# Kernel optimization log

Measured on AMD Instinct MI355X. Metric: run time of the kernel, lower is better.

Reference implementation:

```python
import jax, jax.numpy as jnp
import numpy as np

B, T, KD, QD, AD, VD, W = 16, 4096, 1024, 1024, 512, 1024, 8


def moving_sum(x, back, forward):
    # x: [B, T] -> windowed sum over [t-back, t+forward], matches F.conv1d with ones filter
    xp = jnp.pad(x, ((0, 0), (back, forward)))[:, None, :]
    filt = jnp.ones((1, 1, back + forward + 1), x.dtype)
    y = jax.lax.conv_general_dilated(xp, filt, (1,), 'VALID')
    return y[:, 0, :]


def setup_inputs() -> dict:
    key = jax.random.key(0)
    ks = jax.random.split(key, 16)
    inp = {
        'key': jax.random.normal(ks[0], (B, T, KD), jnp.float32),
        'value': jax.random.normal(ks[1], (B, T, VD), jnp.float32),
        'query': jax.random.normal(ks[2], (B, 1, QD), jnp.float32),
        'noise': jax.random.normal(ks[3], (B, T), jnp.float32),
        'Wk_mono': jax.random.normal(ks[4], (KD, AD), jnp.float32) * (KD ** -0.5),
        'b_mono': jnp.zeros((AD,), jnp.float32),
        'Wq_mono': jax.random.normal(ks[5], (QD, AD), jnp.float32) * (QD ** -0.5),
        'Wk_chunk': jax.random.normal(ks[6], (KD, AD), jnp.float32) * (KD ** -0.5),
        'b_chunk': jnp.zeros((AD,), jnp.float32),
        'Wq_chunk': jax.random.normal(ks[7], (QD, AD), jnp.float32) * (QD ** -0.5),
        'r_mono': jnp.array([-4.0], jnp.float32),
        'r_chunk': jnp.array([-4.0], jnp.float32),
    }
    # weight-normalized v vectors: g = sqrt(1/attn_dim), w = g * v/||v||
    g = (1.0 / AD) ** 0.5
    vm = jax.random.normal(ks[8], (AD,), jnp.float32)
    vc = jax.random.normal(ks[9], (AD,), jnp.float32)
    inp['v_mono'] = g * vm / jnp.linalg.norm(vm)
    inp['v_chunk'] = g * vc / jnp.linalg.norm(vc)
    return inp


def _forward(key, value, query, noise, Wk_mono, b_mono, Wq_mono, v_mono, r_mono,
             Wk_chunk, b_chunk, Wq_chunk, v_chunk, r_chunk):
    bs, kmax = key.shape[0], key.shape[1]
    # aw_prev default: one-hot at position 0
    aw_prev = jnp.zeros((bs, kmax), key.dtype).at[:, 0].set(1.0)

    # monotonic energy: [B, T]
    qm = jnp.einsum('bqd,da->bqa', query, Wq_mono)  # [B,1,A], broadcasts over T
    e_mono = jnp.einsum('bta,a->bt', jnp.tanh(key @ Wk_mono + b_mono + qm), v_mono) + r_mono

    # parallel mode: sigmoid with additive gaussian noise
    p_choose = jax.nn.sigmoid(e_mono + noise)
    # safe_cumprod with the original's exclusive_cumsum (prepends ONES, drops last)
    log1mp = jnp.log(jnp.clip(1.0 - p_choose, 1e-10, 1.0))
    shifted = jnp.concatenate([jnp.ones((bs, 1), key.dtype), log1mp[:, :-1]], axis=1)
    cumprod_1mp = jnp.exp(jnp.cumsum(shifted, axis=1))
    aw = p_choose * cumprod_1mp * jnp.cumsum(
        aw_prev / jnp.clip(cumprod_1mp, 1e-10, 1.0), axis=1)

    # chunk energy
    qc = jnp.einsum('bqd,da->bqa', query, Wq_chunk)
    e_chunk = jnp.einsum('bta,a->bt', jnp.tanh(key @ Wk_chunk + b_chunk + qc), v_chunk) + r_chunk

    # efficient chunkwise attention
    u = e_chunk - jnp.max(e_chunk, axis=1, keepdims=True)
    softmax_exp = jnp.maximum(jnp.exp(u), 1e-5)
    denom = moving_sum(softmax_exp, back=W - 1, forward=0)
    beta = softmax_exp * moving_sum(aw / denom, back=0, forward=W - 1)

    cv = jnp.einsum('bt,btd->bd', beta, value)[:, None, :]  # [B,1,VD]
    return cv, aw[..., None]


def reference(key, value, query, noise, Wk_mono, b_mono, Wq_mono, v_mono, r_mono,
              Wk_chunk, b_chunk, Wq_chunk, v_chunk, r_chunk):
    return _forward(key, value, query, noise, Wk_mono, b_mono, Wq_mono, v_mono, r_mono,
                    Wk_chunk, b_chunk, Wq_chunk, v_chunk, r_chunk)
```

## Files before the change

### kernel.cpp

```cpp
#include <hip/hip_runtime.h>
#include <hip/hip_bf16.h>
#include <math.h>

#define B_   16
#define T_   4096
#define KD_  1024
#define AD_  512
#define VD_  1024

typedef float f32x4 __attribute__((ext_vector_type(4)));
typedef short s16x8 __attribute__((ext_vector_type(8)));

static __device__ __forceinline__ short f2bf(float f) {
    __hip_bfloat16 h = __float2bfloat16(f);
    return __builtin_bit_cast(short, h);
}

static __device__ __forceinline__ float fast_tanh(float x) {
    x = fminf(fmaxf(x, -15.f), 15.f);
    float e = __expf(2.f * x);
    return (e - 1.f) / (e + 1.f);
}

static __device__ __forceinline__ void gload16(const void* g, void* l) {
    __builtin_amdgcn_global_load_lds(
        (const __attribute__((address_space(1))) void*)(g),
        (__attribute__((address_space(3))) void*)(l), 16, 0, 0);
}


__global__ __launch_bounds__(256) void cvt_key_blk_kernel(
    const float* __restrict__ key, short* __restrict__ keyB) {
    const size_t nchunk = (size_t)B_ * T_ * KD_ / 8;
    size_t stride = (size_t)gridDim.x * 256;
    for (size_t g = (size_t)blockIdx.x * 256 + threadIdx.x; g < nchunk; g += stride) {
        const float* p = key + g * 8;
        f32x4 f0 = *reinterpret_cast<const f32x4*>(p);
        f32x4 f1 = *reinterpret_cast<const f32x4*>(p + 4);
        s16x8 h;
        h[0] = f2bf(f0[0]); h[1] = f2bf(f0[1]); h[2] = f2bf(f0[2]); h[3] = f2bf(f0[3]);
        h[4] = f2bf(f1[0]); h[5] = f2bf(f1[1]); h[6] = f2bf(f1[2]); h[7] = f2bf(f1[3]);
        size_t m = g >> 7;
        int kc = (int)(g & 127);
        size_t mt = m >> 7;
        int r = (int)(m & 127);
        int kt = kc >> 2;
        int sub = kc & 3;
        int c = (r << 2) | (sub ^ ((r >> 1) & 3));
        *reinterpret_cast<s16x8*>(keyB + (((mt * 32 + kt) * 512 + c) << 3)) = h;
    }
}

__global__ __launch_bounds__(256) void qproj_kernel(
    const float* __restrict__ query,
    const float* __restrict__ Wq_mono, const float* __restrict__ b_mono,
    const float* __restrict__ Wq_chunk, const float* __restrict__ b_chunk,
    float* __restrict__ qb) {
    __shared__ float red[4][64];
    int b = blockIdx.x;
    int mat = blockIdx.y;
    int ac = blockIdx.z;
    const float* Wq = mat ? Wq_chunk : Wq_mono;
    const float* bb = mat ? b_chunk : b_mono;
    int al = threadIdx.x & 63;
    int dg = threadIdx.x >> 6;
    int a = ac * 64 + al;
    const float* q = query + b * KD_ + dg * 256;
    const float* wp = Wq + (size_t)(dg * 256) * AD_ + a;
    float s = 0.f;
#pragma unroll 4
    for (int d = 0; d < 256; ++d)
        s += q[d] * wp[(size_t)d * AD_];
    red[dg][al] = s;
    __syncthreads();
    if (dg == 0) {
        float t = red[0][al] + red[1][al] + red[2][al] + red[3][al];
        qb[(mat * B_ + b) * AD_ + a] = t + bb[a];
    }
}

__global__ __launch_bounds__(256) void wtrans_kernel(
    const float* __restrict__ Wk_mono, const float* __restrict__ Wk_chunk,
    short* __restrict__ WkT, short* __restrict__ WkTB) {
    __shared__ float tile[32][33];
    int n0 = blockIdx.x * 32;
    int k0 = blockIdx.y * 32;
    int tx = threadIdx.x;
    int ty = threadIdx.y;
    int tid = ty * 32 + tx;
    const float* src;
    int nloc;
    if (n0 < 512) { src = Wk_mono;  nloc = n0; }
    else          { src = Wk_chunk; nloc = n0 - 512; }
#pragma unroll
    for (int i = 0; i < 4; ++i) {
        int k = ty + i * 8;
        tile[k][tx] = src[(size_t)(k0 + k) * AD_ + nloc + tx];
    }
    __syncthreads();
#pragma unroll
    for (int i = 0; i < 4; ++i) {
        int r = ty + i * 8;
        WkT[(size_t)(n0 + r) * KD_ + k0 + tx] = f2bf(tile[tx][r]);
    }
    if (tid < 128) {
        int r = tid >> 2;
        int sub = tid & 3;
        s16x8 h;
#pragma unroll
        for (int j = 0; j < 8; ++j)
            h[j] = f2bf(tile[sub * 8 + j][r]);
        int n = n0 + r;
        int nblk = n >> 7;
        int rloc = n & 127;
        int kt = k0 >> 5;
        int c = (rloc << 2) | (sub ^ ((rloc >> 1) & 3));
        *reinterpret_cast<s16x8*>(WkTB + (((size_t)(nblk * 32 + kt) * 512 + c) << 3)) = h;
    }
}

__global__ __launch_bounds__(256) void gemm_e_bf_kernel(
    const short* __restrict__ keyB,
    const short* __restrict__ WkTB,
    const float* __restrict__ qb,
    const float* __restrict__ v_mono, const float* __restrict__ v_chunk,
    float* __restrict__ e_ws ) {
    __shared__ short As[2][128 * 32];
    __shared__ short Bs[2][128 * 32];
    int tid = threadIdx.x;
    int bid = blockIdx.x;
    int swz = (bid & 7) * 512 + (bid >> 3);
    int mt = swz >> 3;
    int nt = swz & 7;
    int mBase = mt * 128;
    int nBase = nt * 128;
    int lane = tid & 63;
    int wid = tid >> 6;
    int wr = wid >> 1, wc = wid & 1;
    int col16 = lane & 15, g4 = lane >> 4;

    int c0 = wid * 128 + lane;
    int c1 = c0 + 64;
    const short* pA0 = keyB + (((size_t)mt * 32) * 512 + c0) * 8;
    const short* pA1 = keyB + (((size_t)mt * 32) * 512 + c1) * 8;
    const short* pB0 = WkTB + (((size_t)nt * 32) * 512 + c0) * 8;
    const short* pB1 = WkTB + (((size_t)nt * 32) * 512 + c1) * 8;
    int sOff0 = (wid * 128 + 0) * 8;
    int sOff1 = (wid * 128 + 64) * 8;

    int aoff[4], boff[4];
#pragma unroll
    for (int m = 0; m < 4; ++m) {
        int row = wr * 64 + m * 16 + col16;
        aoff[m] = (row * 4 + (g4 ^ ((row >> 1) & 3))) * 8;
    }
#pragma unroll
    for (int n = 0; n < 4; ++n) {
        int row = wc * 64 + n * 16 + col16;
        boff[n] = (row * 4 + (g4 ^ ((row >> 1) & 3))) * 8;
    }

    f32x4 zero4 = {0.f, 0.f, 0.f, 0.f};
    f32x4 acc[4][4];
#pragma unroll
    for (int m = 0; m < 4; ++m)
#pragma unroll
        for (int n = 0; n < 4; ++n) acc[m][n] = zero4;

    gload16(pA0, &As[0][sOff0]);
    gload16(pA1, &As[0][sOff1]);
    gload16(pB0, &Bs[0][sOff0]);
    gload16(pB1, &Bs[0][sOff1]);
    pA0 += 4096; pA1 += 4096; pB0 += 4096; pB1 += 4096;
    __syncthreads();

    int cur = 0;
    for (int kt = 0; kt < 31; ++kt) {
        int nxt = cur ^ 1;
        gload16(pA0, &As[nxt][sOff0]);
        gload16(pA1, &As[nxt][sOff1]);
        gload16(pB0, &Bs[nxt][sOff0]);
        gload16(pB1, &Bs[nxt][sOff1]);
        pA0 += 4096; pA1 += 4096; pB0 += 4096; pB1 += 4096;
        s16x8 af[4], bfr[4];
#pragma unroll
        for (int m = 0; m < 4; ++m)
            af[m] = *reinterpret_cast<const s16x8*>(&As[cur][aoff[m]]);
#pragma unroll
        for (int n = 0; n < 4; ++n)
            bfr[n] = *reinterpret_cast<const s16x8*>(&Bs[cur][boff[n]]);
#pragma unroll
        for (int m = 0; m < 4; ++m)
#pragma unroll
            for (int n = 0; n < 4; ++n)
                acc[m][n] = __builtin_amdgcn_mfma_f32_16x16x32_bf16(af[m], bfr[n], acc[m][n], 0, 0, 0);
        __syncthreads();
        cur = nxt;
    }
    {
        s16x8 af[4], bfr[4];
#pragma unroll
        for (int m = 0; m < 4; ++m)
            af[m] = *reinterpret_cast<const s16x8*>(&As[cur][aoff[m]]);
#pragma unroll
        for (int n = 0; n < 4; ++n)
            bfr[n] = *reinterpret_cast<const s16x8*>(&Bs[cur][boff[n]]);
#pragma unroll
        for (int m = 0; m < 4; ++m)
#pragma unroll
            for (int n = 0; n < 4; ++n)
                acc[m][n] = __builtin_amdgcn_mfma_f32_16x16x32_bf16(af[m], bfr[n], acc[m][n], 0, 0, 0);
    }

    int bIdx = mBase >> 12;
    int matrix = nBase >> 9;
    int aBase = (nBase & 511) + wc * 64 + col16;
    const float* qbRow = qb + (matrix * B_ + bIdx) * AD_;
    const float* vv = matrix ? v_chunk : v_mono;
    float* eArr = e_ws + matrix * (B_ * T_);
    float qcol[4], vcol[4];
#pragma unroll
    for (int n = 0; n < 4; ++n) {
        int a = aBase + n * 16;
        qcol[n] = qbRow[a];
        vcol[n] = vv[a];
    }
#pragma unroll
    for (int m = 0; m < 4; ++m) {
        float s0 = 0.f, s1 = 0.f, s2 = 0.f, s3 = 0.f;
#pragma unroll
        for (int n = 0; n < 4; ++n) {
            s0 += fast_tanh(acc[m][n][0] + qcol[n]) * vcol[n];
            s1 += fast_tanh(acc[m][n][1] + qcol[n]) * vcol[n];
            s2 += fast_tanh(acc[m][n][2] + qcol[n]) * vcol[n];
            s3 += fast_tanh(acc[m][n][3] + qcol[n]) * vcol[n];
        }
#pragma unroll
        for (int mask = 1; mask < 16; mask <<= 1) {
            s0 += __shfl_xor(s0, mask, 64);
            s1 += __shfl_xor(s1, mask, 64);
            s2 += __shfl_xor(s2, mask, 64);
            s3 += __shfl_xor(s3, mask, 64);
        }
        if (col16 == 0) {
            int rowB = mBase + wr * 64 + m * 16 + g4 * 4;
            atomicAdd(&eArr[rowB + 0], s0);
            atomicAdd(&eArr[rowB + 1], s1);
            atomicAdd(&eArr[rowB + 2], s2);
            atomicAdd(&eArr[rowB + 3], s3);
        }
    }
}

__global__ __launch_bounds__(256) void gemm_e_f32a_kernel(
    const float* __restrict__ key,
    const short* __restrict__ WkT,
    const float* __restrict__ qb,
    const float* __restrict__ v_mono, const float* __restrict__ v_chunk,
    float* __restrict__ e_ws) {
    __shared__ short As[128][40];
    __shared__ short Bs[128][40];
    int tid = threadIdx.x;
    int bid = blockIdx.x;
    int mt = bid >> 3;
    int nt = bid & 7;
    int mBase = mt * 128;
    int nBase = nt * 128;
    int lane = tid & 63;
    int wid = tid >> 6;
    int wr = wid >> 1, wc = wid & 1;
    int col16 = lane & 15, g4 = lane >> 4;

    f32x4 zero4 = {0.f, 0.f, 0.f, 0.f};
    f32x4 acc[4][4];
#pragma unroll
    for (int m = 0; m < 4; ++m)
#pragma unroll
        for (int n = 0; n < 4; ++n) acc[m][n] = zero4;

    for (int kt = 0; kt < 32; ++kt) {
        int k0 = kt * 32;
#pragma unroll
        for (int c2 = 0; c2 < 2; ++c2) {
            int c = c2 * 256 + tid;
            int row = c >> 2;
            int kk = (c & 3) * 8;
            const float* srcA = key + (size_t)(mBase + row) * KD_ + k0 + kk;
            f32x4 f0 = *reinterpret_cast<const f32x4*>(srcA);
            f32x4 f1 = *reinterpret_cast<const f32x4*>(srcA + 4);
            s16x8 h;
            h[0] = f2bf(f0[0]); h[1] = f2bf(f0[1]); h[2] = f2bf(f0[2]); h[3] = f2bf(f0[3]);
            h[4] = f2bf(f1[0]); h[5] = f2bf(f1[1]); h[6] = f2bf(f1[2]); h[7] = f2bf(f1[3]);
            *reinterpret_cast<s16x8*>(&As[row][kk]) = h;
            const short* srcB = WkT + (size_t)(nBase + row) * KD_ + k0 + kk;
            *reinterpret_cast<s16x8*>(&Bs[row][kk]) = *reinterpret_cast<const s16x8*>(srcB);
        }
        __syncthreads();
        s16x8 af[4], bfr[4];
#pragma unroll
        for (int m = 0; m < 4; ++m)
            af[m] = *reinterpret_cast<const s16x8*>(&As[wr * 64 + m * 16 + col16][g4 * 8]);
#pragma unroll
        for (int n = 0; n < 4; ++n)
            bfr[n] = *reinterpret_cast<const s16x8*>(&Bs[wc * 64 + n * 16 + col16][g4 * 8]);
#pragma unroll
        for (int m = 0; m < 4; ++m)
#pragma unroll
            for (int n = 0; n < 4; ++n)
                acc[m][n] = __builtin_amdgcn_mfma_f32_16x16x32_bf16(af[m], bfr[n], acc[m][n], 0, 0, 0);
        __syncthreads();
    }

    int bIdx = mBase >> 12;
    int matrix = nBase >> 9;
    int aBase = (nBase & 511) + wc * 64 + col16;
    const float* qbRow = qb + (matrix * B_ + bIdx) * AD_;
    const float* vv = matrix ? v_chunk : v_mono;
    float* eArr = e_ws + matrix * (B_ * T_);
    float qcol[4], vcol[4];
#pragma unroll
    for (int n = 0; n < 4; ++n) {
        int a = aBase + n * 16;
        qcol[n] = qbRow[a];
        vcol[n] = vv[a];
    }
#pragma unroll
    for (int m = 0; m < 4; ++m) {
        float s0 = 0.f, s1 = 0.f, s2 = 0.f, s3 = 0.f;
#pragma unroll
        for (int n = 0; n < 4; ++n) {
            s0 += fast_tanh(acc[m][n][0] + qcol[n]) * vcol[n];
            s1 += fast_tanh(acc[m][n][1] + qcol[n]) * vcol[n];
            s2 += fast_tanh(acc[m][n][2] + qcol[n]) * vcol[n];
            s3 += fast_tanh(acc[m][n][3] + qcol[n]) * vcol[n];
        }
#pragma unroll
        for (int mask = 1; mask < 16; mask <<= 1) {
            s0 += __shfl_xor(s0, mask, 64);
            s1 += __shfl_xor(s1, mask, 64);
            s2 += __shfl_xor(s2, mask, 64);
            s3 += __shfl_xor(s3, mask, 64);
        }
        if (col16 == 0) {
            int rowB = mBase + wr * 64 + m * 16 + g4 * 4;
            atomicAdd(&eArr[rowB + 0], s0);
            atomicAdd(&eArr[rowB + 1], s1);
            atomicAdd(&eArr[rowB + 2], s2);
            atomicAdd(&eArr[rowB + 3], s3);
        }
    }
}

__global__ __launch_bounds__(256) void scan_kernel(
    const float* __restrict__ e_ws,
    const float* __restrict__ noise,
    const float* __restrict__ r_mono, const float* __restrict__ r_chunk,
    float* __restrict__ aw_out, float* __restrict__ beta_out) {
    __shared__ float s_aw[T_];
    __shared__ float s_sexp[T_];
    __shared__ float s_ad[T_];
    __shared__ float s_w[4];
    int b = blockIdx.x;
    int tid = threadIdx.x;
    int lane = tid & 63;
    int wid4 = tid >> 6;
    int t0 = tid * 16;
    const float* em = e_ws + b * T_;
    const float* ec = e_ws + B_ * T_ + b * T_;
    const float* nz = noise + b * T_;
    float rm = r_mono[0], rc = r_chunk[0];

    float pv[16], lp[16];
    float run = 0.f;
#pragma unroll
    for (int j = 0; j < 16; ++j) {
        float x = em[t0 + j] + rm + nz[t0 + j];
        float p = 1.f / (1.f + expf(-x));
        pv[j] = p;
        float om = fminf(fmaxf(1.f - p, 1e-10f), 1.f);
        lp[j] = run;
        run += logf(om);
    }
    float x = run;
#pragma unroll
    for (int off = 1; off < 64; off <<= 1) {
        float y = __shfl_up(x, off, 64);
        if (lane >= off) x += y;
    }
    if (lane == 63) s_w[wid4] = x;
    __syncthreads();
    float wbase = 0.f;
#pragma unroll
    for (int i = 0; i < 3; ++i) if (i < wid4) wbase += s_w[i];
    float base = 1.f + (wbase + x - run);
#pragma unroll
    for (int j = 0; j < 16; ++j) {
        float aw = pv[j] * expf(base + lp[j]);
        s_aw[t0 + j] = aw;
        aw_out[b * T_ + t0 + j] = aw;
    }
    float evs[16];
    float lmax = -INFINITY;
#pragma unroll
    for (int j = 0; j < 16; ++j) {
        float v = ec[t0 + j] + rc;
        evs[j] = v;
        lmax = fmaxf(lmax, v);
    }
#pragma unroll
    for (int off = 1; off < 64; off <<= 1)
        lmax = fmaxf(lmax, __shfl_xor(lmax, off, 64));
    __syncthreads();
    if (lane == 0) s_w[wid4] = lmax;
    __syncthreads();
    float mx = fmaxf(fmaxf(s_w[0], s_w[1]), fmaxf(s_w[2], s_w[3]));
#pragma unroll
    for (int j = 0; j < 16; ++j)
        s_sexp[t0 + j] = fmaxf(expf(evs[j] - mx), 1e-5f);
    __syncthreads();
#pragma unroll
    for (int j = 0; j < 16; ++j) {
        int t = t0 + j;
        int lo = t - 7; if (lo < 0) lo = 0;
        float d = 0.f;
        for (int i = lo; i <= t; ++i) d += s_sexp[i];
        s_ad[t] = s_aw[t] / d;
    }
    __syncthreads();
#pragma unroll
    for (int j = 0; j < 16; ++j) {
        int t = t0 + j;
        int hi = t + 7; if (hi > T_ - 1) hi = T_ - 1;
        float m2 = 0.f;
        for (int i = t; i <= hi; ++i) m2 += s_ad[i];
        beta_out[b * T_ + t] = s_sexp[t] * m2;
    }
}

__global__ __launch_bounds__(256) void cv_kernel(
    const float* __restrict__ value,
    const float* __restrict__ beta,
    float* __restrict__ cv) {
    __shared__ float s_beta[128];
    int b = blockIdx.x;
    int tc = blockIdx.y;
    int tid = threadIdx.x;
    int t0 = tc * 128;
    if (tid < 128) s_beta[tid] = beta[b * T_ + t0 + tid];
    __syncthreads();
    int d0 = tid * 4;
    f32x4 acc = {0.f, 0.f, 0.f, 0.f};
    const float* vp = value + (size_t)(b * T_ + t0) * VD_ + d0;
#pragma unroll 4
    for (int i = 0; i < 128; ++i) {
        f32x4 v = *reinterpret_cast<const f32x4*>(vp + (size_t)i * VD_);
        float bt = s_beta[i];
        acc[0] += bt * v[0];
        acc[1] += bt * v[1];
        acc[2] += bt * v[2];
        acc[3] += bt * v[3];
    }
    atomicAdd(&cv[b * VD_ + d0 + 0], acc[0]);
    atomicAdd(&cv[b * VD_ + d0 + 1], acc[1]);
    atomicAdd(&cv[b * VD_ + d0 + 2], acc[2]);
    atomicAdd(&cv[b * VD_ + d0 + 3], acc[3]);
}

extern "C" void kernel_launch(void* const* d_in, const int* in_sizes, int n_in,
                              void* d_out, int out_size, void* d_ws, size_t ws_size,
                              hipStream_t stream) {
    const float* key      = (const float*)d_in[0];
    const float* value    = (const float*)d_in[1];
    const float* query    = (const float*)d_in[2];
    const float* noise    = (const float*)d_in[3];
    const float* Wk_mono  = (const float*)d_in[4];
    const float* b_mono   = (const float*)d_in[5];
    const float* Wq_mono  = (const float*)d_in[6];
    const float* Wk_chunk = (const float*)d_in[7];
    const float* b_chunk  = (const float*)d_in[8];
    const float* Wq_chunk = (const float*)d_in[9];
    const float* r_mono   = (const float*)d_in[10];
    const float* r_chunk  = (const float*)d_in[11];
    const float* v_mono   = (const float*)d_in[12];
    const float* v_chunk  = (const float*)d_in[13];
    float* out = (float*)d_out;

    char* ws = (char*)d_ws;
    size_t off = 0;
    float* e_ws = (float*)(ws + off); off += 2 * B_ * T_ * sizeof(float);
    float* qb   = (float*)(ws + off); off += 2 * B_ * AD_ * sizeof(float);
    short* WkT  = (short*)(ws + off); off += (size_t)KD_ * KD_ * 2;
    short* WkTB = (short*)(ws + off); off += (size_t)KD_ * KD_ * 2;
    float* beta = (float*)(ws + off); off += B_ * T_ * sizeof(float);
    size_t key_bf_off = off;
    size_t key_bf_bytes = (size_t)B_ * T_ * KD_ * 2;
    bool big_ws = (ws_size >= key_bf_off + key_bf_bytes);
    short* keyB = (short*)(ws + key_bf_off);

    hipMemsetAsync(e_ws, 0, 2 * B_ * T_ * sizeof(float), stream);
    hipMemsetAsync(out, 0, B_ * VD_ * sizeof(float), stream);

    qproj_kernel<<<dim3(16, 2, 8), 256, 0, stream>>>(query, Wq_mono, b_mono, Wq_chunk, b_chunk, qb);
    wtrans_kernel<<<dim3(32, 32), dim3(32, 8), 0, stream>>>(Wk_mono, Wk_chunk, WkT, WkTB);
    if (big_ws) {
        cvt_key_blk_kernel<<<4096, 256, 0, stream>>>(key, keyB);
        gemm_e_bf_kernel<<<4096, 256, 0, stream>>>(keyB, WkTB, qb, v_mono, v_chunk, e_ws);
    } else {
        gemm_e_f32a_kernel<<<4096, 256, 0, stream>>>(key, WkT, qb, v_mono, v_chunk, e_ws);
    }
    scan_kernel<<<16, 256, 0, stream>>>(e_ws, noise, r_mono, r_chunk, out + B_ * VD_, beta);
    cv_kernel<<<dim3(16, 32), 256, 0, stream>>>(value, beta, out);
}
```

Measured before the change: 399.3 us.

## Fuse key fp32-to-bf16 conversion into GEMM loads and drop separate conversion pass

Removes the standalone kernel that converted key to a blocked bf16 copy. The energy GEMM now loads fp32 key rows directly into registers, converts to bf16 and writes swizzled LDS, overlapping with the MFMA loop. This eliminates a full write and reread of a large bf16 key buffer. In exchange, each block reads twice the A bytes from memory or L2, and the A tile goes through registers instead of async global-to-LDS loads. The unused transposed weight copy and the fallback GEMM are also removed.

```diff
diff --git a/kernel.cpp b/kernel.cpp
--- a/kernel.cpp
+++ b/kernel.cpp
@@ -28,28 +28,6 @@
         (__attribute__((address_space(3))) void*)(l), 16, 0, 0);
 }
 
-
-__global__ __launch_bounds__(256) void cvt_key_blk_kernel(
-    const float* __restrict__ key, short* __restrict__ keyB) {
-    const size_t nchunk = (size_t)B_ * T_ * KD_ / 8;
-    size_t stride = (size_t)gridDim.x * 256;
-    for (size_t g = (size_t)blockIdx.x * 256 + threadIdx.x; g < nchunk; g += stride) {
-        const float* p = key + g * 8;
-        f32x4 f0 = *reinterpret_cast<const f32x4*>(p);
-        f32x4 f1 = *reinterpret_cast<const f32x4*>(p + 4);
-        s16x8 h;
-        h[0] = f2bf(f0[0]); h[1] = f2bf(f0[1]); h[2] = f2bf(f0[2]); h[3] = f2bf(f0[3]);
-        h[4] = f2bf(f1[0]); h[5] = f2bf(f1[1]); h[6] = f2bf(f1[2]); h[7] = f2bf(f1[3]);
-        size_t m = g >> 7;
-        int kc = (int)(g & 127);
-        size_t mt = m >> 7;
-        int r = (int)(m & 127);
-        int kt = kc >> 2;
-        int sub = kc & 3;
-        int c = (r << 2) | (sub ^ ((r >> 1) & 3));
-        *reinterpret_cast<s16x8*>(keyB + (((mt * 32 + kt) * 512 + c) << 3)) = h;
-    }
-}
 
 __global__ __launch_bounds__(256) void qproj_kernel(
     const float* __restrict__ query,
@@ -81,7 +59,7 @@
 
 __global__ __launch_bounds__(256) void wtrans_kernel(
     const float* __restrict__ Wk_mono, const float* __restrict__ Wk_chunk,
-    short* __restrict__ WkT, short* __restrict__ WkTB) {
+    short* __restrict__ WkTB) {
     __shared__ float tile[32][33];
     int n0 = blockIdx.x * 32;
     int k0 = blockIdx.y * 32;
@@ -98,11 +76,6 @@
         tile[k][tx] = src[(size_t)(k0 + k) * AD_ + nloc + tx];
     }
     __syncthreads();
-#pragma unroll
-    for (int i = 0; i < 4; ++i) {
-        int r = ty + i * 8;
-        WkT[(size_t)(n0 + r) * KD_ + k0 + tx] = f2bf(tile[tx][r]);
-    }
     if (tid < 128) {
         int r = tid >> 2;
         int sub = tid & 3;
@@ -119,8 +92,8 @@
     }
 }
 
-__global__ __launch_bounds__(256) void gemm_e_bf_kernel(
-    const short* __restrict__ keyB,
+__global__ __launch_bounds__(256) void gemm_e_kernel(
+    const float* __restrict__ key,
     const short* __restrict__ WkTB,
     const float* __restrict__ qb,
     const float* __restrict__ v_mono, const float* __restrict__ v_chunk,
@@ -141,13 +114,18 @@
 
     int c0 = wid * 128 + lane;
     int c1 = c0 + 64;
-    const short* pA0 = keyB + (((size_t)mt * 32) * 512 + c0) * 8;
-    const short* pA1 = keyB + (((size_t)mt * 32) * 512 + c1) * 8;
     const short* pB0 = WkTB + (((size_t)nt * 32) * 512 + c0) * 8;
     const short* pB1 = WkTB + (((size_t)nt * 32) * 512 + c1) * 8;
     int sOff0 = (wid * 128 + 0) * 8;
     int sOff1 = (wid * 128 + 64) * 8;
 
+    int arow = tid >> 1;
+    int ad0 = (tid & 1) * 2;
+    const float* pA = key + (size_t)(mBase + arow) * KD_ + ad0 * 8;
+    int aswz = (arow >> 1) & 3;
+    int aslot0 = (arow * 4 + (ad0 ^ aswz)) * 8;
+    int aslot1 = (arow * 4 + ((ad0 + 1) ^ aswz)) * 8;
+
     int aoff[4], boff[4];
 #pragma unroll
     for (int m = 0; m < 4; ++m) {
@@ -167,21 +145,36 @@
 #pragma unroll
         for (int n = 0; n < 4; ++n) acc[m][n] = zero4;
 
-    gload16(pA0, &As[0][sOff0]);
-    gload16(pA1, &As[0][sOff1]);
     gload16(pB0, &Bs[0][sOff0]);
     gload16(pB1, &Bs[0][sOff1]);
-    pA0 += 4096; pA1 += 4096; pB0 += 4096; pB1 += 4096;
+    pB0 += 4096; pB1 += 4096;
+    {
+        f32x4 q0 = *reinterpret_cast<const f32x4*>(pA);
+        f32x4 q1 = *reinterpret_cast<const f32x4*>(pA + 4);
+        f32x4 q2 = *reinterpret_cast<const f32x4*>(pA + 8);
+        f32x4 q3 = *reinterpret_cast<const f32x4*>(pA + 12);
+        s16x8 h0, h1;
+        h0[0]=f2bf(q0[0]); h0[1]=f2bf(q0[1]); h0[2]=f2bf(q0[2]); h0[3]=f2bf(q0[3]);
+        h0[4]=f2bf(q1[0]); h0[5]=f2bf(q1[1]); h0[6]=f2bf(q1[2]); h0[7]=f2bf(q1[3]);
+        h1[0]=f2bf(q2[0]); h1[1]=f2bf(q2[1]); h1[2]=f2bf(q2[2]); h1[3]=f2bf(q2[3]);
+        h1[4]=f2bf(q3[0]); h1[5]=f2bf(q3[1]); h1[6]=f2bf(q3[2]); h1[7]=f2bf(q3[3]);
+        *reinterpret_cast<s16x8*>(&As[0][aslot0]) = h0;
+        *reinterpret_cast<s16x8*>(&As[0][aslot1]) = h1;
+    }
+    const float* pAn = pA + 32;
     __syncthreads();
 
     int cur = 0;
     for (int kt = 0; kt < 31; ++kt) {
         int nxt = cur ^ 1;
-        gload16(pA0, &As[nxt][sOff0]);
-        gload16(pA1, &As[nxt][sOff1]);
         gload16(pB0, &Bs[nxt][sOff0]);
         gload16(pB1, &Bs[nxt][sOff1]);
-        pA0 += 4096; pA1 += 4096; pB0 += 4096; pB1 += 4096;
+        pB0 += 4096; pB1 += 4096;
+        f32x4 q0 = *reinterpret_cast<const f32x4*>(pAn);
+        f32x4 q1 = *reinterpret_cast<const f32x4*>(pAn + 4);
+        f32x4 q2 = *reinterpret_cast<const f32x4*>(pAn + 8);
+        f32x4 q3 = *reinterpret_cast<const f32x4*>(pAn + 12);
+        pAn += 32;
         s16x8 af[4], bfr[4];
 #pragma unroll
         for (int m = 0; m < 4; ++m)
@@ -194,6 +187,13 @@
 #pragma unroll
             for (int n = 0; n < 4; ++n)
                 acc[m][n] = __builtin_amdgcn_mfma_f32_16x16x32_bf16(af[m], bfr[n], acc[m][n], 0, 0, 0);
+        s16x8 h0, h1;
+        h0[0]=f2bf(q0[0]); h0[1]=f2bf(q0[1]); h0[2]=f2bf(q0[2]); h0[3]=f2bf(q0[3]);
+        h0[4]=f2bf(q1[0]); h0[5]=f2bf(q1[1]); h0[6]=f2bf(q1[2]); h0[7]=f2bf(q1[3]);
+        h1[0]=f2bf(q2[0]); h1[1]=f2bf(q2[1]); h1[2]=f2bf(q2[2]); h1[3]=f2bf(q2[3]);
+        h1[4]=f2bf(q3[0]); h1[5]=f2bf(q3[1]); h1[6]=f2bf(q3[2]); h1[7]=f2bf(q3[3]);
+        *reinterpret_cast<s16x8*>(&As[nxt][aslot0]) = h0;
+        *reinterpret_cast<s16x8*>(&As[nxt][aslot1]) = h1;
         __syncthreads();
         cur = nxt;
     }
@@ -210,105 +210,6 @@
 #pragma unroll
             for (int n = 0; n < 4; ++n)
                 acc[m][n] = __builtin_amdgcn_mfma_f32_16x16x32_bf16(af[m], bfr[n], acc[m][n], 0, 0, 0);
-    }
-
-    int bIdx = mBase >> 12;
-    int matrix = nBase >> 9;
-    int aBase = (nBase & 511) + wc * 64 + col16;
-    const float* qbRow = qb + (matrix * B_ + bIdx) * AD_;
-    const float* vv = matrix ? v_chunk : v_mono;
-    float* eArr = e_ws + matrix * (B_ * T_);
-    float qcol[4], vcol[4];
-#pragma unroll
-    for (int n = 0; n < 4; ++n) {
-        int a = aBase + n * 16;
-        qcol[n] = qbRow[a];
-        vcol[n] = vv[a];
-    }
-#pragma unroll
-    for (int m = 0; m < 4; ++m) {
-        float s0 = 0.f, s1 = 0.f, s2 = 0.f, s3 = 0.f;
-#pragma unroll
-        for (int n = 0; n < 4; ++n) {
-            s0 += fast_tanh(acc[m][n][0] + qcol[n]) * vcol[n];
-            s1 += fast_tanh(acc[m][n][1] + qcol[n]) * vcol[n];
-            s2 += fast_tanh(acc[m][n][2] + qcol[n]) * vcol[n];
-            s3 += fast_tanh(acc[m][n][3] + qcol[n]) * vcol[n];
-        }
-#pragma unroll
-        for (int mask = 1; mask < 16; mask <<= 1) {
-            s0 += __shfl_xor(s0, mask, 64);
-            s1 += __shfl_xor(s1, mask, 64);
-            s2 += __shfl_xor(s2, mask, 64);
-            s3 += __shfl_xor(s3, mask, 64);
-        }
-        if (col16 == 0) {
-            int rowB = mBase + wr * 64 + m * 16 + g4 * 4;
-            atomicAdd(&eArr[rowB + 0], s0);
-            atomicAdd(&eArr[rowB + 1], s1);
-            atomicAdd(&eArr[rowB + 2], s2);
-            atomicAdd(&eArr[rowB + 3], s3);
-        }
-    }
-}
-
-__global__ __launch_bounds__(256) void gemm_e_f32a_kernel(
-    const float* __restrict__ key,
-    const short* __restrict__ WkT,
-    const float* __restrict__ qb,
-    const float* __restrict__ v_mono, const float* __restrict__ v_chunk,
-    float* __restrict__ e_ws) {
-    __shared__ short As[128][40];
-    __shared__ short Bs[128][40];
-    int tid = threadIdx.x;
-    int bid = blockIdx.x;
-    int mt = bid >> 3;
-    int nt = bid & 7;
-    int mBase = mt * 128;
-    int nBase = nt * 128;
-    int lane = tid & 63;
-    int wid = tid >> 6;
-    int wr = wid >> 1, wc = wid & 1;
-    int col16 = lane & 15, g4 = lane >> 4;
-
-    f32x4 zero4 = {0.f, 0.f, 0.f, 0.f};
-    f32x4 acc[4][4];
-#pragma unroll
-    for (int m = 0; m < 4; ++m)
-#pragma unroll
-        for (int n = 0; n < 4; ++n) acc[m][n] = zero4;
-
-    for (int kt = 0; kt < 32; ++kt) {
-        int k0 = kt * 32;
-#pragma unroll
-        for (int c2 = 0; c2 < 2; ++c2) {
-            int c = c2 * 256 + tid;
-            int row = c >> 2;
-            int kk = (c & 3) * 8;
-            const float* srcA = key + (size_t)(mBase + row) * KD_ + k0 + kk;
-            f32x4 f0 = *reinterpret_cast<const f32x4*>(srcA);
-            f32x4 f1 = *reinterpret_cast<const f32x4*>(srcA + 4);
-            s16x8 h;
-            h[0] = f2bf(f0[0]); h[1] = f2bf(f0[1]); h[2] = f2bf(f0[2]); h[3] = f2bf(f0[3]);
-            h[4] = f2bf(f1[0]); h[5] = f2bf(f1[1]); h[6] = f2bf(f1[2]); h[7] = f2bf(f1[3]);
-            *reinterpret_cast<s16x8*>(&As[row][kk]) = h;
-            const short* srcB = WkT + (size_t)(nBase + row) * KD_ + k0 + kk;
-            *reinterpret_cast<s16x8*>(&Bs[row][kk]) = *reinterpret_cast<const s16x8*>(srcB);
-        }
-        __syncthreads();
-        s16x8 af[4], bfr[4];
-#pragma unroll
-        for (int m = 0; m < 4; ++m)
-            af[m] = *reinterpret_cast<const s16x8*>(&As[wr * 64 + m * 16 + col16][g4 * 8]);
-#pragma unroll
-        for (int n = 0; n < 4; ++n)
-            bfr[n] = *reinterpret_cast<const s16x8*>(&Bs[wc * 64 + n * 16 + col16][g4 * 8]);
-#pragma unroll
-        for (int m = 0; m < 4; ++m)
-#pragma unroll
-            for (int n = 0; n < 4; ++n)
-                acc[m][n] = __builtin_amdgcn_mfma_f32_16x16x32_bf16(af[m], bfr[n], acc[m][n], 0, 0, 0);
-        __syncthreads();
     }
 
     int bIdx = mBase >> 12;
@@ -489,25 +390,15 @@
     size_t off = 0;
     float* e_ws = (float*)(ws + off); off += 2 * B_ * T_ * sizeof(float);
     float* qb   = (float*)(ws + off); off += 2 * B_ * AD_ * sizeof(float);
-    short* WkT  = (short*)(ws + off); off += (size_t)KD_ * KD_ * 2;
     short* WkTB = (short*)(ws + off); off += (size_t)KD_ * KD_ * 2;
     float* beta = (float*)(ws + off); off += B_ * T_ * sizeof(float);
-    size_t key_bf_off = off;
-    size_t key_bf_bytes = (size_t)B_ * T_ * KD_ * 2;
-    bool big_ws = (ws_size >= key_bf_off + key_bf_bytes);
-    short* keyB = (short*)(ws + key_bf_off);
 
     hipMemsetAsync(e_ws, 0, 2 * B_ * T_ * sizeof(float), stream);
     hipMemsetAsync(out, 0, B_ * VD_ * sizeof(float), stream);
 
     qproj_kernel<<<dim3(16, 2, 8), 256, 0, stream>>>(query, Wq_mono, b_mono, Wq_chunk, b_chunk, qb);
-    wtrans_kernel<<<dim3(32, 32), dim3(32, 8), 0, stream>>>(Wk_mono, Wk_chunk, WkT, WkTB);
-    if (big_ws) {
-        cvt_key_blk_kernel<<<4096, 256, 0, stream>>>(key, keyB);
-        gemm_e_bf_kernel<<<4096, 256, 0, stream>>>(keyB, WkTB, qb, v_mono, v_chunk, e_ws);
-    } else {
-        gemm_e_f32a_kernel<<<4096, 256, 0, stream>>>(key, WkT, qb, v_mono, v_chunk, e_ws);
-    }
+    wtrans_kernel<<<dim3(32, 32), dim3(32, 8), 0, stream>>>(Wk_mono, Wk_chunk, WkTB);
+    gemm_e_kernel<<<4096, 256, 0, stream>>>(key, WkTB, qb, v_mono, v_chunk, e_ws);
     scan_kernel<<<16, 256, 0, stream>>>(e_ws, noise, r_mono, r_chunk, out + B_ * VD_, beta);
     cv_kernel<<<dim3(16, 32), 256, 0, stream>>>(value, beta, out);
 }
```

After: 392.6 us. Within noise of the previous version (-1.7%).
